# Kernel tuning notes

Measured on AMD Instinct MI355X. Metric: run time of the kernel, lower is better.

Reference implementation:

```python
import jax, jax.numpy as jnp
import numpy as np

EMBED = 256
HEADS = 8
SR = 2
RED = 2


def setup_inputs() -> dict:
    key = jax.random.key(0)
    ks = jax.random.split(key, 12)
    N, B, C = 1024, 64, EMBED
    inp = {
        "query": jax.random.normal(ks[0], (N, B, C), jnp.float32),
        "H": 32,
        "W": 32,
        "key": jax.random.normal(ks[1], (N, B, C), jnp.float32),
        "value": jax.random.normal(ks[2], (N, B, C), jnp.float32),
        # parameters
        "in_proj_weight": jax.random.normal(ks[3], (3 * C, C), jnp.float32) * (1.0 / np.sqrt(C)),
        "in_proj_bias": jnp.zeros((3 * C,), jnp.float32),
        "sr_w": jax.random.normal(ks[4], (C, C, SR, SR), jnp.float32) * np.sqrt(2.0 / (SR * SR * C)),
        "sr_b": jnp.zeros((C,), jnp.float32),
        "norm_g": jnp.ones((C,), jnp.float32),
        "norm_b": jnp.zeros((C,), jnp.float32),
        "out_w": jax.random.normal(ks[5], (C, C), jnp.float32) * (1.0 / np.sqrt(C)),
        "out_b": jnp.zeros((C,), jnp.float32),
        "se_w1": jax.random.normal(ks[6], (C // RED, C), jnp.float32) * 0.02,
        "se_w2": jax.random.normal(ks[7], (C, C // RED), jnp.float32) * 0.02,
    }
    return inp


def _angles(H, W):
    # get_index: a = (pi/2)*(i//W)/H, b = (pi/2)*(i%W)/W for flattened row-major index
    c = np.pi / 2
    idx = jnp.arange(H * W)
    a = c * (idx // W).astype(jnp.float32) / H
    b = c * (idx % W).astype(jnp.float32) / W
    return a, b


def _layernorm(x, g, b, eps=1e-5):
    mu = jnp.mean(x, -1, keepdims=True)
    var = jnp.mean(jnp.square(x - mu), -1, keepdims=True)
    return (x - mu) * jax.lax.rsqrt(var + eps) * g + b


def _abs_clamp(t, lo=1e-4, hi=1e4):
    return jnp.clip(jnp.abs(t), lo, hi) * jnp.sign(t)


def reference(query, H, W, key, value, in_proj_weight, in_proj_bias, sr_w, sr_b,
              norm_g, norm_b, out_w, out_b, se_w1, se_w2):
    N, B, C = query.shape
    h = HEADS
    hd = C // h
    scaling = hd ** (-0.5)

    x = jnp.transpose(query, (1, 0, 2))  # (B, N, C)

    # squeeze-excite gate from query: mean over tokens -> fc1 -> relu -> fc2 -> sigmoid
    se = jnp.mean(x, axis=1)                       # (B, C)
    se = jax.nn.sigmoid(jax.nn.relu(se @ se_w1.T) @ se_w2.T)  # (B, C)

    # spatial reduction conv (kernel=stride=sr_ratio) + layernorm for k/v source
    x_img = jnp.transpose(x, (0, 2, 1)).reshape(B, C, H, W)
    xr = jax.lax.conv_general_dilated(
        x_img, sr_w, window_strides=(SR, SR), padding="VALID",
        dimension_numbers=("NCHW", "OIHW", "NCHW"))
    xr = xr + sr_b[None, :, None, None]
    Hs, Ws = H // SR, W // SR
    Ns = Hs * Ws
    xr = jnp.transpose(xr.reshape(B, C, Ns), (0, 2, 1))  # (B, Ns, C)
    xr = _layernorm(xr, norm_g, norm_b)

    Wq, Wk, Wv = in_proj_weight[:C], in_proj_weight[C:2 * C], in_proj_weight[2 * C:]
    bq, bk, bv = in_proj_bias[:C], in_proj_bias[C:2 * C], in_proj_bias[2 * C:]

    def split_heads(t):  # (B, L, C) -> (B*h, L, hd)
        Bb, L, _ = t.shape
        return jnp.transpose(t.reshape(Bb, L, h, hd), (0, 2, 1, 3)).reshape(Bb * h, L, hd)

    q = split_heads((x @ Wq.T + bq) * scaling)
    k = split_heads(xr @ Wk.T + bk)
    v = split_heads(xr @ Wv.T + bv)

    q = jax.nn.relu(q)
    k = jax.nn.relu(k)

    # cosFormer-2d "sum" reweighting: cos(a_i - a_j) + cos(b_i - b_j)
    a, b = _angles(H, W)       # (N,)
    a2, b2 = _angles(Hs, Ws)   # (Ns,)

    def reweight(t, aa, bb):  # (BH, L, hd), angles (L,) -> (BH, L, 4*hd)
        aa = aa[None, :, None]
        bb = bb[None, :, None]
        return jnp.concatenate(
            [t * jnp.cos(aa), t * jnp.sin(aa), t * jnp.cos(bb), t * jnp.sin(bb)], axis=-1)

    q_ = reweight(q, a, b)     # (BH, N, 4hd)
    k_ = reweight(k, a2, b2)   # (BH, Ns, 4hd)

    # linear attention: never materialize the NxNs matrix
    kv = jnp.einsum("bnd,bnm->bdm", k_, v)             # (BH, 4hd, hd)
    denom = jnp.einsum("bnd,bd->bn", q_, k_.sum(1))    # (BH, N)
    denom = _abs_clamp(denom)
    attn = jnp.einsum("bnd,bdm->bnm", q_, kv) / denom[..., None]  # (BH, N, hd)

    attn = jnp.transpose(attn.reshape(B, h, N, hd), (0, 2, 1, 3)).reshape(B, N, C)
    out = attn @ out_w.T + out_b            # (B, N, C)
    out = out * se[:, None, :]              # SE channel gating
    return jnp.transpose(out, (1, 0, 2))    # (N, B, C)
```

## Files before the change

### kernel.cpp

```cpp
#include <hip/hip_runtime.h>

#define NTOK 1024
#define NB   64
#define CD   256
#define NHEAD 8
#define HDIM 32
#define NS 256
#define NBC 16384

typedef __attribute__((ext_vector_type(8))) short short8v;
typedef __attribute__((ext_vector_type(4))) short short4v;
typedef __attribute__((ext_vector_type(4))) float f32x4;

__device__ __forceinline__ unsigned bfr(float x){
  unsigned u = __float_as_uint(x);
  return (u + 0x7fffu + ((u>>16)&1u)) >> 16;
}
__device__ __forceinline__ void split2(float x, short &h, short &l){
  unsigned hu = bfr(x);
  float hf = __uint_as_float(hu << 16);
  unsigned lu = bfr(x - hf);
  h = (short)hu; l = (short)lu;
}

__global__ __launch_bounds__(256) void k_wcvt(const float* __restrict__ ipw, const float* __restrict__ ow,
                                              const float* __restrict__ srw,
                                              short* __restrict__ Wih, short* __restrict__ Wil,
                                              short* __restrict__ Woh, short* __restrict__ Wol,
                                              short* __restrict__ Wsh, short* __restrict__ Wsl){
  int u = blockIdx.x*256 + threadIdx.x;
  float xs[8];
  short* dh; short* dl; int dof;
  if (u < 24576){
    int n = u >> 5, off = (u & 31)*8;
    const float* s = ipw + n*CD + off;
    #pragma unroll
    for (int i=0;i<8;++i) xs[i] = s[i];
    dh = Wih; dl = Wil; dof = n*CD + off;
  } else if (u < 32768){
    int v = u - 24576;
    int n = v >> 5, off = (v & 31)*8;
    const float* s = ow + n*CD + off;
    #pragma unroll
    for (int i=0;i<8;++i) xs[i] = s[i];
    dh = Woh; dl = Wol; dof = n*CD + off;
  } else {
    int v = u - 32768;
    int n = v >> 7, koff = (v & 127)*8;
    int g = koff >> 8, cin0 = koff & 255;
    #pragma unroll
    for (int i=0;i<8;++i) xs[i] = srw[n*1024 + (cin0+i)*4 + g];
    dh = Wsh; dl = Wsl; dof = n*1024 + koff;
  }
  short8v h, l;
  #pragma unroll
  for (int i=0;i<8;++i){ short a,b; split2(xs[i],a,b); h[i]=a; l[i]=b; }
  *(short8v*)(dh + dof) = h;
  *(short8v*)(dl + dof) = l;
}

__global__ __launch_bounds__(256) void k_trig(float* __restrict__ t1, float* __restrict__ t2){
  int n = blockIdx.x*256 + threadIdx.x;
  const float c = 1.57079632679489662f;
  float aa = c * (float)(n >> 5) / 32.0f;
  float bb = c * (float)(n & 31) / 32.0f;
  t1[n*4+0]=cosf(aa); t1[n*4+1]=sinf(aa); t1[n*4+2]=cosf(bb); t1[n*4+3]=sinf(bb);
  if (n < 256){
    float a2 = c * (float)(n >> 4) / 16.0f;
    float b2 = c * (float)(n & 15) / 16.0f;
    t2[n*4+0]=cosf(a2); t2[n*4+1]=sinf(a2); t2[n*4+2]=cosf(b2); t2[n*4+3]=sinf(b2);
  }
}

__global__ __launch_bounds__(256) void k_semean(const float* __restrict__ q, float* __restrict__ part){
  int b = blockIdx.x >> 2, qr = blockIdx.x & 3;
  int c = threadIdx.x;
  const float* qp = q + (qr*256)*NBC + b*CD + c;
  float s0=0.f,s1=0.f,s2=0.f,s3=0.f;
  for (int n=0;n<256;n+=4){
    s0 += qp[(n  )*NBC];
    s1 += qp[(n+1)*NBC];
    s2 += qp[(n+2)*NBC];
    s3 += qp[(n+3)*NBC];
  }
  part[blockIdx.x*256 + c] = (s0+s1)+(s2+s3);
}

__global__ __launch_bounds__(256) void k_semlp(const float* __restrict__ part, const float* __restrict__ w1,
                                               const float* __restrict__ w2, float* __restrict__ se){
  __shared__ float sm[256];
  __shared__ float s1s[128];
  int b = blockIdx.x, t = threadIdx.x;
  float s = (part[(b*4+0)*256+t]+part[(b*4+1)*256+t])+(part[(b*4+2)*256+t]+part[(b*4+3)*256+t]);
  sm[t] = s*(1.0f/1024.0f);
  __syncthreads();
  if (t < 128){
    float a = 0.f;
    const float* wr = w1 + t*256;
    for (int c=0;c<256;c+=4){
      float4 wf = *(const float4*)(wr+c);
      a += sm[c]*wf.x + sm[c+1]*wf.y + sm[c+2]*wf.z + sm[c+3]*wf.w;
    }
    s1s[t] = fmaxf(a, 0.f);
  }
  __syncthreads();
  float a = 0.f;
  const float* wr2 = w2 + t*128;
  for (int c=0;c<128;c+=4){
    float4 wf = *(const float4*)(wr2+c);
    a += s1s[c]*wf.x + s1s[c+1]*wf.y + s1s[c+2]*wf.z + s1s[c+3]*wf.w;
  }
  se[b*256+t] = 1.0f/(1.0f+expf(-a));
}

__global__ __launch_bounds__(256) void k_conv(const float* __restrict__ qf,
                                              const short* __restrict__ Wsh, const short* __restrict__ Wsl,
                                              const float* __restrict__ srb, float* __restrict__ xr){
  __shared__ __align__(16) short Ah[64*32];
  __shared__ __align__(16) short Al[64*32];
  __shared__ __align__(16) short Bh[128*32];
  __shared__ __align__(16) short Bl[128*32];
  int mblk = blockIdx.x >> 1, nblk = blockIdx.x & 1;
  int m0 = mblk*64, n0 = nblk*128;
  int b = mblk >> 2;
  int pos0 = m0 & 255;
  int t = threadIdx.x, wave = t>>6, lane = t&63;
  int wm = wave>>1, wn = wave&1;
  int q = lane>>4, r = lane&15;
  int ra = t>>2, pa = (t&3)*8;
  int posA = pos0 + ra, hs = posA>>4, ws2 = posA&15;
  const f32x4 fz = {0.f,0.f,0.f,0.f};
  f32x4 acc[2][4];
  #pragma unroll
  for (int s=0;s<2;++s)
    #pragma unroll
    for (int tt=0;tt<4;++tt) acc[s][tt] = fz;
  for (int kc=0; kc<32; ++kc){
    int g = kc>>3, cin0 = (kc&7)*32;
    int gh = g>>1, gw = g&1;
    int tok = (2*hs+gh)*32 + 2*ws2 + gw;
    const float* src = qf + (size_t)tok*NBC + b*CD + cin0 + pa;
    float4 fa = *(const float4*)src;
    float4 fb = *(const float4*)(src+4);
    float xs[8] = {fa.x,fa.y,fa.z,fa.w,fb.x,fb.y,fb.z,fb.w};
    short8v hh, ll;
    #pragma unroll
    for (int i=0;i<8;++i){ short a0,b0; split2(xs[i],a0,b0); hh[i]=a0; ll[i]=b0; }
    *(short8v*)(Ah + ra*32 + pa) = hh;
    *(short8v*)(Al + ra*32 + pa) = ll;
    int ko = kc*32;
    #pragma unroll
    for (int rep=0; rep<2; ++rep){
      int rr = ra + rep*64;
      int gb = (n0 + rr)*1024 + ko + pa;
      *(short8v*)(Bh + rr*32 + pa) = *(const short8v*)(Wsh + gb);
      *(short8v*)(Bl + rr*32 + pa) = *(const short8v*)(Wsl + gb);
    }
    __syncthreads();
    short8v ah[2], al[2];
    #pragma unroll
    for (int s=0;s<2;++s){
      int row = wm*32 + s*16 + r;
      ah[s] = *(const short8v*)(Ah + row*32 + q*8);
      al[s] = *(const short8v*)(Al + row*32 + q*8);
    }
    #pragma unroll
    for (int tt=0;tt<4;++tt){
      int brow = wn*64 + tt*16 + r;
      short8v bh = *(const short8v*)(Bh + brow*32 + q*8);
      short8v bl = *(const short8v*)(Bl + brow*32 + q*8);
      #pragma unroll
      for (int s=0;s<2;++s){
        acc[s][tt] = __builtin_amdgcn_mfma_f32_16x16x32_bf16(ah[s], bh, acc[s][tt], 0,0,0);
        acc[s][tt] = __builtin_amdgcn_mfma_f32_16x16x32_bf16(ah[s], bl, acc[s][tt], 0,0,0);
        acc[s][tt] = __builtin_amdgcn_mfma_f32_16x16x32_bf16(al[s], bh, acc[s][tt], 0,0,0);
      }
    }
    __syncthreads();
  }
  #pragma unroll
  for (int s=0;s<2;++s){
    #pragma unroll
    for (int tt=0;tt<4;++tt){
      int c = n0 + wn*64 + tt*16 + r;
      float bias = srb[c];
      #pragma unroll
      for (int i=0;i<4;++i){
        int m = m0 + wm*32 + s*16 + q*4 + i;
        xr[m*CD + c] = acc[s][tt][i] + bias;
      }
    }
  }
}

__global__ __launch_bounds__(256) void k_ln(const float* __restrict__ xr, const float* __restrict__ g,
                                            const float* __restrict__ bta, short* __restrict__ Xh,
                                            short* __restrict__ Xl){
  int wv = threadIdx.x >> 6, lane = threadIdx.x & 63;
  int row = blockIdx.x*4 + wv;
  float4 v = ((const float4*)(xr + row*CD))[lane];
  float s = (v.x+v.y)+(v.z+v.w);
  #pragma unroll
  for (int off=1; off<64; off<<=1) s += __shfl_xor(s, off, 64);
  float mu = s * (1.0f/256.0f);
  float dx=v.x-mu, dy=v.y-mu, dz=v.z-mu, dw=v.w-mu;
  float s2 = (dx*dx+dy*dy)+(dz*dz+dw*dw);
  #pragma unroll
  for (int off=1; off<64; off<<=1) s2 += __shfl_xor(s2, off, 64);
  float inv = 1.0f / sqrtf(s2*(1.0f/256.0f) + 1e-5f);
  float4 gr = ((const float4*)g)[lane];
  float4 br = ((const float4*)bta)[lane];
  float o0 = dx*inv*gr.x + br.x;
  float o1 = dy*inv*gr.y + br.y;
  float o2 = dz*inv*gr.z + br.z;
  float o3 = dw*inv*gr.w + br.w;
  short4v h, l; short a0,b0;
  split2(o0,a0,b0); h[0]=a0; l[0]=b0;
  split2(o1,a0,b0); h[1]=a0; l[1]=b0;
  split2(o2,a0,b0); h[2]=a0; l[2]=b0;
  split2(o3,a0,b0); h[3]=a0; l[3]=b0;
  *(short4v*)(Xh + row*CD + lane*4) = h;
  *(short4v*)(Xl + row*CD + lane*4) = l;
}

__global__ __launch_bounds__(256) void k_qproj(const float* __restrict__ qf,
                                               const short* __restrict__ Wih, const short* __restrict__ Wil,
                                               const float* __restrict__ ipb,
                                               short* __restrict__ Qbh, short* __restrict__ Qbl){
  __shared__ __align__(16) short smem[16384];
  short* Ah = smem;
  short* Al = smem + 4096;
  short* Bh = smem + 8192;
  short* Bl = smem + 12288;
  int mblk = blockIdx.x >> 1, nblk = blockIdx.x & 1;
  int m0 = mblk*128, n0 = nblk*128;
  int t = threadIdx.x, wave = t>>6, lane = t&63;
  int wm = wave>>1, wn = wave&1;
  int q = lane>>4, r = lane&15;
  int cr = t>>2, cp = (t&3)*8;
  int cpS = (((t&3) ^ ((cr>>1)&3)))*8;
  int sw8 = ((r>>1)&3)*8;
  const f32x4 fz = {0.f,0.f,0.f,0.f};
  f32x4 acc[4][4];
  #pragma unroll
  for (int s=0;s<4;++s)
    #pragma unroll
    for (int tt=0;tt<4;++tt) acc[s][tt] = fz;
  for (int kc=0; kc<8; ++kc){
    int ko = kc*32;
    #pragma unroll
    for (int rep=0; rep<2; ++rep){
      int rr = cr + rep*64;
      int m = m0 + rr;
      const float* src = qf + (size_t)(m & 1023)*NBC + (m >> 10)*CD + ko + cp;
      float4 fa = *(const float4*)src;
      float4 fb = *(const float4*)(src+4);
      float xs[8] = {fa.x,fa.y,fa.z,fa.w,fb.x,fb.y,fb.z,fb.w};
      short8v hh, ll;
      #pragma unroll
      for (int i=0;i<8;++i){ short a0,b0; split2(xs[i],a0,b0); hh[i]=a0; ll[i]=b0; }
      *(short8v*)(Ah + rr*32 + cpS) = hh;
      *(short8v*)(Al + rr*32 + cpS) = ll;
      int gb = (n0 + rr)*CD + ko + cp;
      *(short8v*)(Bh + rr*32 + cpS) = *(const short8v*)(Wih + gb);
      *(short8v*)(Bl + rr*32 + cpS) = *(const short8v*)(Wil + gb);
    }
    __syncthreads();
    short8v ah[4], al[4];
    #pragma unroll
    for (int s=0;s<4;++s){
      int row = wm*64 + s*16 + r;
      ah[s] = *(const short8v*)(Ah + row*32 + ((q*8)^sw8));
      al[s] = *(const short8v*)(Al + row*32 + ((q*8)^sw8));
    }
    #pragma unroll
    for (int tt=0;tt<4;++tt){
      int brow = wn*64 + tt*16 + r;
      short8v bh = *(const short8v*)(Bh + brow*32 + ((q*8)^sw8));
      short8v bl = *(const short8v*)(Bl + brow*32 + ((q*8)^sw8));
      #pragma unroll
      for (int s=0;s<4;++s){
        acc[s][tt] = __builtin_amdgcn_mfma_f32_16x16x32_bf16(ah[s], bh, acc[s][tt], 0,0,0);
        acc[s][tt] = __builtin_amdgcn_mfma_f32_16x16x32_bf16(ah[s], bl, acc[s][tt], 0,0,0);
        acc[s][tt] = __builtin_amdgcn_mfma_f32_16x16x32_bf16(al[s], bh, acc[s][tt], 0,0,0);
      }
    }
    __syncthreads();
  }
  const float sc = 0.17677669529663687f;
  short* T = smem;
  #pragma unroll
  for (int s=0;s<4;++s){
    #pragma unroll
    for (int tt=0;tt<4;++tt){
      int c_loc = wn*64 + tt*16 + r;
      int chunk = c_loc >> 3, cb = c_loc & 7;
      float bias = ipb[n0 + c_loc];
      #pragma unroll
      for (int i=0;i<4;++i){
        int m_loc = wm*64 + s*16 + q*4 + i;
        float val = fmaxf(acc[s][tt][i] + bias, 0.f)*sc;
        unsigned hu = bfr(val);
        T[m_loc*128 + ((chunk ^ (m_loc&7))<<3) + cb] = (short)hu;
        acc[s][tt][i] = val - __uint_as_float(hu<<16);
      }
    }
  }
  __syncthreads();
  {
    int mrl = (lane>>2);
    int ccl = lane&3;
    #pragma unroll
    for (int e=0;e<8;++e){
      int hl = e&3, mg = e>>2;
      int m_loc = wave*32 + mg*16 + mrl;
      int cc16 = hl*4 + ccl;
      short8v v = *(const short8v*)(T + m_loc*128 + ((cc16 ^ (m_loc&7))<<3));
      *(short8v*)(Qbh + ((size_t)((n0>>5)+hl))*2097152 + (size_t)(m0+m_loc)*32 + ccl*8) = v;
    }
  }
  __syncthreads();
  #pragma unroll
  for (int s=0;s<4;++s){
    #pragma unroll
    for (int tt=0;tt<4;++tt){
      int c_loc = wn*64 + tt*16 + r;
      int chunk = c_loc >> 3, cb = c_loc & 7;
      #pragma unroll
      for (int i=0;i<4;++i){
        int m_loc = wm*64 + s*16 + q*4 + i;
        T[m_loc*128 + ((chunk ^ (m_loc&7))<<3) + cb] = (short)bfr(acc[s][tt][i]);
      }
    }
  }
  __syncthreads();
  {
    int mrl = (lane>>2);
    int ccl = lane&3;
    #pragma unroll
    for (int e=0;e<8;++e){
      int hl = e&3, mg = e>>2;
      int m_loc = wave*32 + mg*16 + mrl;
      int cc16 = hl*4 + ccl;
      short8v v = *(const short8v*)(T + m_loc*128 + ((cc16 ^ (m_loc&7))<<3));
      *(short8v*)(Qbl + ((size_t)((n0>>5)+hl))*2097152 + (size_t)(m0+m_loc)*32 + ccl*8) = v;
    }
  }
}

__global__ __launch_bounds__(256) void k_kvproj(const short* __restrict__ Xh, const short* __restrict__ Xl,
                                                const short* __restrict__ Wkh, const short* __restrict__ Wkl,
                                                const float* __restrict__ ipb, float* __restrict__ kb,
                                                float* __restrict__ vb){
  __shared__ __align__(16) short Ah[128*32];
  __shared__ __align__(16) short Al[128*32];
  __shared__ __align__(16) short Bh[128*32];
  __shared__ __align__(16) short Bl[128*32];
  int mblk = blockIdx.x >> 2, nblk = blockIdx.x & 3;
  int m0 = mblk*128, n0 = nblk*128;
  int t = threadIdx.x, wave = t>>6, lane = t&63;
  int wm = wave>>1, wn = wave&1;
  int q = lane>>4, r = lane&15;
  int cr = t>>2, cp = (t&3)*8;
  const f32x4 fz = {0.f,0.f,0.f,0.f};
  f32x4 acc[4][4];
  #pragma unroll
  for (int s=0;s<4;++s)
    #pragma unroll
    for (int tt=0;tt<4;++tt) acc[s][tt] = fz;
  for (int kc=0; kc<8; ++kc){
    int ko = kc*32;
    #pragma unroll
    for (int rep=0; rep<2; ++rep){
      int rr = cr + rep*64;
      int ga = (m0 + rr)*CD + ko + cp;
      *(short8v*)(Ah + rr*32 + cp) = *(const short8v*)(Xh + ga);
      *(short8v*)(Al + rr*32 + cp) = *(const short8v*)(Xl + ga);
      int gb = (n0 + rr)*CD + ko + cp;
      *(short8v*)(Bh + rr*32 + cp) = *(const short8v*)(Wkh + gb);
      *(short8v*)(Bl + rr*32 + cp) = *(const short8v*)(Wkl + gb);
    }
    __syncthreads();
    short8v ah[4], al[4];
    #pragma unroll
    for (int s=0;s<4;++s){
      int row = wm*64 + s*16 + r;
      ah[s] = *(const short8v*)(Ah + row*32 + q*8);
      al[s] = *(const short8v*)(Al + row*32 + q*8);
    }
    #pragma unroll
    for (int tt=0;tt<4;++tt){
      int brow = wn*64 + tt*16 + r;
      short8v bh = *(const short8v*)(Bh + brow*32 + q*8);
      short8v bl = *(const short8v*)(Bl + brow*32 + q*8);
      #pragma unroll
      for (int s=0;s<4;++s){
        acc[s][tt] = __builtin_amdgcn_mfma_f32_16x16x32_bf16(ah[s], bh, acc[s][tt], 0,0,0);
        acc[s][tt] = __builtin_amdgcn_mfma_f32_16x16x32_bf16(ah[s], bl, acc[s][tt], 0,0,0);
        acc[s][tt] = __builtin_amdgcn_mfma_f32_16x16x32_bf16(al[s], bh, acc[s][tt], 0,0,0);
      }
    }
    __syncthreads();
  }
  #pragma unroll
  for (int s=0;s<4;++s){
    #pragma unroll
    for (int tt=0;tt<4;++tt){
      int c = n0 + wn*64 + tt*16 + r;
      float bias = ipb[256 + c];
      #pragma unroll
      for (int i=0;i<4;++i){
        int m = m0 + wm*64 + s*16 + q*4 + i;
        float v = acc[s][tt][i] + bias;
        if (c < 256) kb[m*CD + c] = fmaxf(v, 0.f);
        else         vb[m*CD + (c-256)] = v;
      }
    }
  }
}

__global__ __launch_bounds__(256) void k_kv(const float* __restrict__ kb, const float* __restrict__ vbuf,
                                            const float* __restrict__ t2, short* __restrict__ Bhp,
                                            short* __restrict__ Blp){
  int bh = blockIdx.x; int b = bh >> 3, h = bh & 7;
  int t = threadIdx.x; int jq = t >> 5, m = t & 31;
  float acc[4][4];
  #pragma unroll
  for (int p=0;p<4;++p){ acc[p][0]=0.f; acc[p][1]=0.f; acc[p][2]=0.f; acc[p][3]=0.f; }
  const float* kbase = kb + h*HDIM + jq*4;
  const float* vbase = vbuf + h*HDIM + m;
  for (int n=0;n<256;++n){
    int ro = (b*NS + n)*CD;
    float4 k4 = *(const float4*)(kbase + ro);
    float vv = vbase[ro];
    float4 tt = *(const float4*)(t2 + n*4);
    float tv[4] = {tt.x, tt.y, tt.z, tt.w};
    float kk[4] = {k4.x, k4.y, k4.z, k4.w};
    #pragma unroll
    for (int p=0;p<4;++p){
      float tp = tv[p]*vv;
      #pragma unroll
      for (int jj=0;jj<4;++jj) acc[p][jj] += tp*kk[jj];
    }
  }
  short* bhb = Bhp + bh*4608;
  short* blb = Blp + bh*4608;
  #pragma unroll
  for (int p=0;p<4;++p){
    short4v h4, l4;
    #pragma unroll
    for (int jj=0;jj<4;++jj){ short a,bq; split2(acc[p][jj],a,bq); h4[jj]=a; l4[jj]=bq; }
    *(short4v*)(bhb + (p*32+m)*32 + jq*4) = h4;
    *(short4v*)(blb + (p*32+m)*32 + jq*4) = l4;
  }
  if (t < 128){
    int p = t >> 5, j = t & 31;
    float s=0.f;
    const float* kp = kb + h*HDIM + j;
    for (int n=0;n<256;++n) s += t2[n*4+p]*kp[(b*NS+n)*CD];
    short a,bq; split2(s,a,bq);
    bhb[(128+p)*32 + j] = a;
    blb[(128+p)*32 + j] = bq;
  } else {
    int idx = t - 128;
    #pragma unroll
    for (int ii=0;ii<3;++ii){
      bhb[4224 + idx*3 + ii] = 0;
      blb[4224 + idx*3 + ii] = 0;
    }
  }
}

__global__ __launch_bounds__(256) void k_attn(const short* __restrict__ Qbh, const short* __restrict__ Qbl,
                                              const short* __restrict__ Bhg, const short* __restrict__ Blg,
                                              const float* __restrict__ t1,
                                              short* __restrict__ Ath, short* __restrict__ Atl){
  __shared__ __align__(16) short Bh[144*32];
  __shared__ __align__(16) short Bl[144*32];
  __shared__ __align__(16) short Ah[256*32];
  __shared__ __align__(16) short Al[256*32];
  int bh = blockIdx.x, b = bh>>3, h = bh&7;
  int t = threadIdx.x, lane = t&63, wave = t>>6;
  int q = lane>>4, r = lane&15;
  {
    const short8v* sh = (const short8v*)(Bhg + bh*4608);
    const short8v* sl = (const short8v*)(Blg + bh*4608);
    for (int i=t; i<576; i+=256){
      ((short8v*)Bh)[i] = sh[i];
      ((short8v*)Bl)[i] = sl[i];
    }
  }
  __syncthreads();
  short8v bf_h[9], bf_l[9];
  #pragma unroll
  for (int nt=0; nt<9; ++nt){
    int row = nt*16 + r;
    bf_h[nt] = *(const short8v*)(Bh + row*32 + q*8);
    bf_l[nt] = *(const short8v*)(Bl + row*32 + q*8);
  }
  const short* qh_base = Qbh + ((size_t)h*65536 + (size_t)b*1024)*32;
  const short* ql_base = Qbl + ((size_t)h*65536 + (size_t)b*1024)*32;
  const f32x4 fz = {0.f,0.f,0.f,0.f};
  for (int u=0; u<4; ++u){
    __syncthreads();
    {
      const short8v* sh = (const short8v*)(qh_base + (u*256 + t)*32);
      const short8v* sl = (const short8v*)(ql_base + (u*256 + t)*32);
      short8v* dh = (short8v*)(Ah + t*32);
      short8v* dl = (short8v*)(Al + t*32);
      #pragma unroll
      for (int i=0;i<4;++i){ dh[i]=sh[i]; dl[i]=sl[i]; }
    }
    __syncthreads();
    #pragma unroll
    for (int mi=0; mi<4; ++mi){
      int mt = wave*4 + mi;
      short8v ah = *(const short8v*)(Ah + (mt*16 + r)*32 + q*8);
      short8v al = *(const short8v*)(Al + (mt*16 + r)*32 + q*8);
      f32x4 acc[9];
      #pragma unroll
      for (int nt=0;nt<9;++nt) acc[nt]=fz;
      #pragma unroll
      for (int nt=0;nt<9;++nt){
        acc[nt] = __builtin_amdgcn_mfma_f32_16x16x32_bf16(ah, bf_h[nt], acc[nt],0,0,0);
        acc[nt] = __builtin_amdgcn_mfma_f32_16x16x32_bf16(ah, bf_l[nt], acc[nt],0,0,0);
        acc[nt] = __builtin_amdgcn_mfma_f32_16x16x32_bf16(al, bf_h[nt], acc[nt],0,0,0);
      }
      int nbase = u*256 + mt*16 + q*4;
      int src = lane & 48;
      #pragma unroll
      for (int i=0;i<4;++i){
        int n = nbase + i;
        float4 tv = *(const float4*)(t1 + n*4);
        float dp0 = __shfl(acc[8][i], src+0, 64);
        float dp1 = __shfl(acc[8][i], src+1, 64);
        float dp2 = __shfl(acc[8][i], src+2, 64);
        float dp3 = __shfl(acc[8][i], src+3, 64);
        float den = tv.x*dp0 + tv.y*dp1 + tv.z*dp2 + tv.w*dp3;
        float a0 = tv.x*acc[0][i] + tv.y*acc[2][i] + tv.z*acc[4][i] + tv.w*acc[6][i];
        float a1 = tv.x*acc[1][i] + tv.y*acc[3][i] + tv.z*acc[5][i] + tv.w*acc[7][i];
        float sgn = (den>0.f) ? 1.f : ((den<0.f)? -1.f : 0.f);
        float ad = fminf(fmaxf(fabsf(den), 1e-4f), 1e4f);
// ... 54 lines not shown
    #pragma unroll
    for (int tt=0;tt<4;++tt){
      int brow = wn*64 + tt*16 + r;
      short8v bh = *(const short8v*)(Bh + brow*32 + q*8);
      short8v bl = *(const short8v*)(Bl + brow*32 + q*8);
      #pragma unroll
      for (int s=0;s<4;++s){
        acc[s][tt] = __builtin_amdgcn_mfma_f32_16x16x32_bf16(ah[s], bh, acc[s][tt], 0,0,0);
        acc[s][tt] = __builtin_amdgcn_mfma_f32_16x16x32_bf16(ah[s], bl, acc[s][tt], 0,0,0);
        acc[s][tt] = __builtin_amdgcn_mfma_f32_16x16x32_bf16(al[s], bh, acc[s][tt], 0,0,0);
      }
    }
    __syncthreads();
  }
  #pragma unroll
  for (int s=0;s<4;++s){
    #pragma unroll
    for (int tt=0;tt<4;++tt){
      int c = n0 + wn*64 + tt*16 + r;
      float bias = obv[c];
      #pragma unroll
      for (int i=0;i<4;++i){
        int m = m0 + wm*64 + s*16 + q*4 + i;
        int bb = m >> 10, ntok = m & 1023;
        float sev = se[bb*CD + c];
        dout[(ntok*NB + bb)*CD + c] = (acc[s][tt][i] + bias)*sev;
      }
    }
  }
}

extern "C" void kernel_launch(void* const* d_in, const int* in_sizes, int n_in,
                              void* d_out, int out_size, void* d_ws, size_t ws_size,
                              hipStream_t stream) {
  const float* query = (const float*)d_in[0];
  const float* ipw = (const float*)d_in[5];
  const float* ipb = (const float*)d_in[6];
  const float* srw = (const float*)d_in[7];
  const float* srb = (const float*)d_in[8];
  const float* ng  = (const float*)d_in[9];
  const float* nbb = (const float*)d_in[10];
  const float* ow  = (const float*)d_in[11];
  const float* obv = (const float*)d_in[12];
  const float* sw1 = (const float*)d_in[13];
  const float* sw2 = (const float*)d_in[14];
  float* dout = (float*)d_out;
  float* ws = (float*)d_ws;

  short* Qbh  = (short*)ws;
  short* Qbl  = (short*)(ws + 8388608);
  float* R1   = ws + 16777216;
  float* kb   = R1;
  float* vb   = R1 + 4194304;
  short* Ath  = (short*)R1;
  short* Atl  = (short*)(R1 + 8388608);
  float* xr   = ws + 33554432;
  short* Xh   = (short*)(ws + 37748736);
  short* Xl   = (short*)(ws + 39845888);
  short* kvbh = (short*)(ws + 41943040);
  short* kvbl = (short*)(ws + 43122688);
  float* part = ws + 44302336;
  float* se   = ws + 44367872;
  float* t1   = ws + 44384256;
  float* t2   = ws + 44388352;
  short* Wih  = (short*)(ws + 44389376);
  short* Wil  = (short*)(ws + 44487680);
  short* Woh  = (short*)(ws + 44585984);
  short* Wol  = (short*)(ws + 44618752);
  short* Wsh  = (short*)(ws + 44651520);
  short* Wsl  = (short*)(ws + 44782592);

  k_wcvt  <<<256,  256,0,stream>>>(ipw, ow, srw, Wih, Wil, Woh, Wol, Wsh, Wsl);
  k_trig  <<<4,    256,0,stream>>>(t1, t2);
  k_semean<<<256,  256,0,stream>>>(query, part);
  k_semlp <<<64,   256,0,stream>>>(part, sw1, sw2, se);
  k_conv  <<<512,  256,0,stream>>>(query, Wsh, Wsl, srb, xr);
  k_ln    <<<4096, 256,0,stream>>>(xr, ng, nbb, Xh, Xl);
  k_qproj <<<1024, 256,0,stream>>>(query, Wih, Wil, ipb, Qbh, Qbl);
  k_kvproj<<<512,  256,0,stream>>>(Xh, Xl, Wih + 256*CD, Wil + 256*CD, ipb, kb, vb);
  k_kv    <<<512,  256,0,stream>>>(kb, vb, t2, kvbh, kvbl);
  k_attn  <<<512,  256,0,stream>>>(Qbh, Qbl, kvbh, kvbl, t1, Ath, Atl);
  k_outproj<<<1024,256,0,stream>>>(Ath, Atl, Woh, Wol, obv, se, dout);
}
```

Before: 458.3 us.

## Merge independent kernels into combined launches and fuse kv build into attention

Groups the independent stages (weight conversion, trig tables, SE mean) into one launch, and the conv, Q projection and SE MLP into another, using block-index dispatch. The kv-state computation now runs inside the attention kernel and writes straight to shared memory, which removes a global round trip and one launch. Workspace buffers are remapped so Ath/Atl no longer alias kb/vb, since those are now read in the same kernel. Block-index dispatch gives each launch a mix of very different block types and shared-memory sizes, which can hurt occupancy and load balance.

```diff
diff --git a/kernel.cpp b/kernel.cpp
--- a/kernel.cpp
+++ b/kernel.cpp
@@ -23,173 +23,300 @@
   h = (short)hu; l = (short)lu;
 }
 
-__global__ __launch_bounds__(256) void k_wcvt(const float* __restrict__ ipw, const float* __restrict__ ow,
-                                              const float* __restrict__ srw,
-                                              short* __restrict__ Wih, short* __restrict__ Wil,
-                                              short* __restrict__ Woh, short* __restrict__ Wol,
-                                              short* __restrict__ Wsh, short* __restrict__ Wsl){
-  int u = blockIdx.x*256 + threadIdx.x;
-  float xs[8];
-  short* dh; short* dl; int dof;
-  if (u < 24576){
-    int n = u >> 5, off = (u & 31)*8;
-    const float* s = ipw + n*CD + off;
-    #pragma unroll
-    for (int i=0;i<8;++i) xs[i] = s[i];
-    dh = Wih; dl = Wil; dof = n*CD + off;
-  } else if (u < 32768){
-    int v = u - 24576;
-    int n = v >> 5, off = (v & 31)*8;
-    const float* s = ow + n*CD + off;
-    #pragma unroll
-    for (int i=0;i<8;++i) xs[i] = s[i];
-    dh = Woh; dl = Wol; dof = n*CD + off;
+__global__ __launch_bounds__(256) void k_pre(const float* __restrict__ ipw, const float* __restrict__ ow,
+                                             const float* __restrict__ srw,
+                                             short* __restrict__ Wih, short* __restrict__ Wil,
+                                             short* __restrict__ Woh, short* __restrict__ Wol,
+                                             short* __restrict__ Wsh, short* __restrict__ Wsl,
+                                             float* __restrict__ t1, float* __restrict__ t2,
+                                             const float* __restrict__ query, float* __restrict__ part){
+  int bid = blockIdx.x, t = threadIdx.x;
+  if (bid < 256){
+    int u = bid*256 + t;
+    float xs[8];
+    short* dh; short* dl; int dof;
+    if (u < 24576){
+      int n = u >> 5, off = (u & 31)*8;
+      const float* s = ipw + n*CD + off;
+      #pragma unroll
+      for (int i=0;i<8;++i) xs[i] = s[i];
+      dh = Wih; dl = Wil; dof = n*CD + off;
+    } else if (u < 32768){
+      int v = u - 24576;
+      int n = v >> 5, off = (v & 31)*8;
+      const float* s = ow + n*CD + off;
+      #pragma unroll
+      for (int i=0;i<8;++i) xs[i] = s[i];
+      dh = Woh; dl = Wol; dof = n*CD + off;
+    } else {
+      int v = u - 32768;
+      int n = v >> 7, koff = (v & 127)*8;
+      int g = koff >> 8, cin0 = koff & 255;
+      #pragma unroll
+      for (int i=0;i<8;++i) xs[i] = srw[n*1024 + (cin0+i)*4 + g];
+      dh = Wsh; dl = Wsl; dof = n*1024 + koff;
+    }
+    short8v h, l;
+    #pragma unroll
+    for (int i=0;i<8;++i){ short a,b; split2(xs[i],a,b); h[i]=a; l[i]=b; }
+    *(short8v*)(dh + dof) = h;
+    *(short8v*)(dl + dof) = l;
+  } else if (bid < 260){
+    int n = (bid-256)*256 + t;
+    const float c = 1.57079632679489662f;
+    float aa = c * (float)(n >> 5) / 32.0f;
+    float bb = c * (float)(n & 31) / 32.0f;
+    t1[n*4+0]=cosf(aa); t1[n*4+1]=sinf(aa); t1[n*4+2]=cosf(bb); t1[n*4+3]=sinf(bb);
+    if (n < 256){
+      float a2 = c * (float)(n >> 4) / 16.0f;
+      float b2 = c * (float)(n & 15) / 16.0f;
+      t2[n*4+0]=cosf(a2); t2[n*4+1]=sinf(a2); t2[n*4+2]=cosf(b2); t2[n*4+3]=sinf(b2);
+    }
   } else {
-    int v = u - 32768;
-    int n = v >> 7, koff = (v & 127)*8;
-    int g = koff >> 8, cin0 = koff & 255;
-    #pragma unroll
-    for (int i=0;i<8;++i) xs[i] = srw[n*1024 + (cin0+i)*4 + g];
-    dh = Wsh; dl = Wsl; dof = n*1024 + koff;
-  }
-  short8v h, l;
-  #pragma unroll
-  for (int i=0;i<8;++i){ short a,b; split2(xs[i],a,b); h[i]=a; l[i]=b; }
-  *(short8v*)(dh + dof) = h;
-  *(short8v*)(dl + dof) = l;
-}
-
-__global__ __launch_bounds__(256) void k_trig(float* __restrict__ t1, float* __restrict__ t2){
-  int n = blockIdx.x*256 + threadIdx.x;
-  const float c = 1.57079632679489662f;
-  float aa = c * (float)(n >> 5) / 32.0f;
-  float bb = c * (float)(n & 31) / 32.0f;
-  t1[n*4+0]=cosf(aa); t1[n*4+1]=sinf(aa); t1[n*4+2]=cosf(bb); t1[n*4+3]=sinf(bb);
-  if (n < 256){
-    float a2 = c * (float)(n >> 4) / 16.0f;
-    float b2 = c * (float)(n & 15) / 16.0f;
-    t2[n*4+0]=cosf(a2); t2[n*4+1]=sinf(a2); t2[n*4+2]=cosf(b2); t2[n*4+3]=sinf(b2);
-  }
-}
-
-__global__ __launch_bounds__(256) void k_semean(const float* __restrict__ q, float* __restrict__ part){
-  int b = blockIdx.x >> 2, qr = blockIdx.x & 3;
-  int c = threadIdx.x;
-  const float* qp = q + (qr*256)*NBC + b*CD + c;
-  float s0=0.f,s1=0.f,s2=0.f,s3=0.f;
-  for (int n=0;n<256;n+=4){
-    s0 += qp[(n  )*NBC];
-    s1 += qp[(n+1)*NBC];
-    s2 += qp[(n+2)*NBC];
-    s3 += qp[(n+3)*NBC];
-  }
-  part[blockIdx.x*256 + c] = (s0+s1)+(s2+s3);
-}
-
-__global__ __launch_bounds__(256) void k_semlp(const float* __restrict__ part, const float* __restrict__ w1,
-                                               const float* __restrict__ w2, float* __restrict__ se){
-  __shared__ float sm[256];
-  __shared__ float s1s[128];
-  int b = blockIdx.x, t = threadIdx.x;
-  float s = (part[(b*4+0)*256+t]+part[(b*4+1)*256+t])+(part[(b*4+2)*256+t]+part[(b*4+3)*256+t]);
-  sm[t] = s*(1.0f/1024.0f);
-  __syncthreads();
-  if (t < 128){
+    int vb_ = bid - 260;
+    int b = vb_ >> 2, qr = vb_ & 3;
+    const float* qp = query + (qr*256)*NBC + b*CD + t;
+    float s0=0.f,s1=0.f,s2=0.f,s3=0.f;
+    for (int n=0;n<256;n+=4){
+      s0 += qp[(n  )*NBC];
+      s1 += qp[(n+1)*NBC];
+      s2 += qp[(n+2)*NBC];
+      s3 += qp[(n+3)*NBC];
+    }
+    part[vb_*256 + t] = (s0+s1)+(s2+s3);
+  }
+}
+
+__global__ __launch_bounds__(256) void k_mid(const float* __restrict__ qf,
+                                             const short* __restrict__ Wsh, const short* __restrict__ Wsl,
+                                             const float* __restrict__ srb, float* __restrict__ xr,
+                                             const short* __restrict__ Wih, const short* __restrict__ Wil,
+                                             const float* __restrict__ ipb,
+                                             short* __restrict__ Qbh, short* __restrict__ Qbl,
+                                             const float* __restrict__ part, const float* __restrict__ w1,
+                                             const float* __restrict__ w2, float* __restrict__ se){
+  __shared__ __align__(16) short smem[16384];
+  int bid = blockIdx.x, t = threadIdx.x;
+  if (bid < 512){
+    short* Ah = smem;
+    short* Al = smem + 2048;
+    short* Bh = smem + 4096;
+    short* Bl = smem + 8192;
+    int mblk = bid >> 1, nblk = bid & 1;
+    int m0 = mblk*64, n0 = nblk*128;
+    int b = mblk >> 2;
+    int pos0 = m0 & 255;
+    int wave = t>>6, lane = t&63;
+    int wm = wave>>1, wn = wave&1;
+    int q = lane>>4, r = lane&15;
+    int ra = t>>2, pa = (t&3)*8;
+    int posA = pos0 + ra, hs = posA>>4, ws2 = posA&15;
+    const f32x4 fz = {0.f,0.f,0.f,0.f};
+    f32x4 acc[2][4];
+    #pragma unroll
+    for (int s=0;s<2;++s)
+      #pragma unroll
+      for (int tt=0;tt<4;++tt) acc[s][tt] = fz;
+    for (int kc=0; kc<32; ++kc){
+      int g = kc>>3, cin0 = (kc&7)*32;
+      int gh = g>>1, gw = g&1;
+      int tok = (2*hs+gh)*32 + 2*ws2 + gw;
+      const float* src = qf + (size_t)tok*NBC + b*CD + cin0 + pa;
+      float4 fa = *(const float4*)src;
+      float4 fb = *(const float4*)(src+4);
+      float xs[8] = {fa.x,fa.y,fa.z,fa.w,fb.x,fb.y,fb.z,fb.w};
+      short8v hh, ll;
+      #pragma unroll
+      for (int i=0;i<8;++i){ short a0,b0; split2(xs[i],a0,b0); hh[i]=a0; ll[i]=b0; }
+      *(short8v*)(Ah + ra*32 + pa) = hh;
+      *(short8v*)(Al + ra*32 + pa) = ll;
+      int ko = kc*32;
+      #pragma unroll
+      for (int rep=0; rep<2; ++rep){
+        int rr = ra + rep*64;
+        int gb = (n0 + rr)*1024 + ko + pa;
+        *(short8v*)(Bh + rr*32 + pa) = *(const short8v*)(Wsh + gb);
+        *(short8v*)(Bl + rr*32 + pa) = *(const short8v*)(Wsl + gb);
+      }
+      __syncthreads();
+      short8v ah[2], al[2];
+      #pragma unroll
+      for (int s=0;s<2;++s){
+        int row = wm*32 + s*16 + r;
+        ah[s] = *(const short8v*)(Ah + row*32 + q*8);
+        al[s] = *(const short8v*)(Al + row*32 + q*8);
+      }
+      #pragma unroll
+      for (int tt=0;tt<4;++tt){
+        int brow = wn*64 + tt*16 + r;
+        short8v bh = *(const short8v*)(Bh + brow*32 + q*8);
+        short8v bl = *(const short8v*)(Bl + brow*32 + q*8);
+        #pragma unroll
+        for (int s=0;s<2;++s){
+          acc[s][tt] = __builtin_amdgcn_mfma_f32_16x16x32_bf16(ah[s], bh, acc[s][tt], 0,0,0);
+          acc[s][tt] = __builtin_amdgcn_mfma_f32_16x16x32_bf16(ah[s], bl, acc[s][tt], 0,0,0);
+          acc[s][tt] = __builtin_amdgcn_mfma_f32_16x16x32_bf16(al[s], bh, acc[s][tt], 0,0,0);
+        }
+      }
+      __syncthreads();
+    }
+    #pragma unroll
+    for (int s=0;s<2;++s){
+      #pragma unroll
+      for (int tt=0;tt<4;++tt){
+        int c = n0 + wn*64 + tt*16 + r;
+        float bias = srb[c];
+        #pragma unroll
+        for (int i=0;i<4;++i){
+          int m = m0 + wm*32 + s*16 + q*4 + i;
+          xr[m*CD + c] = acc[s][tt][i] + bias;
+        }
+      }
+    }
+  } else if (bid < 1536){
+    short* Ah = smem;
+    short* Al = smem + 4096;
+    short* Bh = smem + 8192;
+    short* Bl = smem + 12288;
+    int qb_ = bid - 512;
+    int mblk = qb_ >> 1, nblk = qb_ & 1;
+    int m0 = mblk*128, n0 = nblk*128;
+    int wave = t>>6, lane = t&63;
+    int wm = wave>>1, wn = wave&1;
+    int q = lane>>4, r = lane&15;
+    int cr = t>>2, cp = (t&3)*8;
+    int cpS = (((t&3) ^ ((cr>>1)&3)))*8;
+    int sw8 = ((r>>1)&3)*8;
+    const f32x4 fz = {0.f,0.f,0.f,0.f};
+    f32x4 acc[4][4];
+    #pragma unroll
+    for (int s=0;s<4;++s)
+      #pragma unroll
+      for (int tt=0;tt<4;++tt) acc[s][tt] = fz;
+    for (int kc=0; kc<8; ++kc){
+      int ko = kc*32;
+      #pragma unroll
+      for (int rep=0; rep<2; ++rep){
+        int rr = cr + rep*64;
+        int m = m0 + rr;
+        const float* src = qf + (size_t)(m & 1023)*NBC + (m >> 10)*CD + ko + cp;
+        float4 fa = *(const float4*)src;
+        float4 fb = *(const float4*)(src+4);
+        float xs[8] = {fa.x,fa.y,fa.z,fa.w,fb.x,fb.y,fb.z,fb.w};
+        short8v hh, ll;
+        #pragma unroll
+        for (int i=0;i<8;++i){ short a0,b0; split2(xs[i],a0,b0); hh[i]=a0; ll[i]=b0; }
+        *(short8v*)(Ah + rr*32 + cpS) = hh;
+        *(short8v*)(Al + rr*32 + cpS) = ll;
+        int gb = (n0 + rr)*CD + ko + cp;
+        *(short8v*)(Bh + rr*32 + cpS) = *(const short8v*)(Wih + gb);
+        *(short8v*)(Bl + rr*32 + cpS) = *(const short8v*)(Wil + gb);
+      }
+      __syncthreads();
+      short8v ah[4], al[4];
+      #pragma unroll
+      for (int s=0;s<4;++s){
+        int row = wm*64 + s*16 + r;
+        ah[s] = *(const short8v*)(Ah + row*32 + ((q*8)^sw8));
+        al[s] = *(const short8v*)(Al + row*32 + ((q*8)^sw8));
+      }
+      #pragma unroll
+      for (int tt=0;tt<4;++tt){
+        int brow = wn*64 + tt*16 + r;
+        short8v bh = *(const short8v*)(Bh + brow*32 + ((q*8)^sw8));
+        short8v bl = *(const short8v*)(Bl + brow*32 + ((q*8)^sw8));
+        #pragma unroll
+        for (int s=0;s<4;++s){
+          acc[s][tt] = __builtin_amdgcn_mfma_f32_16x16x32_bf16(ah[s], bh, acc[s][tt], 0,0,0);
+          acc[s][tt] = __builtin_amdgcn_mfma_f32_16x16x32_bf16(ah[s], bl, acc[s][tt], 0,0,0);
+          acc[s][tt] = __builtin_amdgcn_mfma_f32_16x16x32_bf16(al[s], bh, acc[s][tt], 0,0,0);
+        }
+      }
+      __syncthreads();
+    }
+    const float sc = 0.17677669529663687f;
+    short* T = smem;
+    #pragma unroll
+    for (int s=0;s<4;++s){
+      #pragma unroll
+      for (int tt=0;tt<4;++tt){
+        int c_loc = wn*64 + tt*16 + r;
+        int chunk = c_loc >> 3, cb = c_loc & 7;
+        float bias = ipb[n0 + c_loc];
+        #pragma unroll
+        for (int i=0;i<4;++i){
+          int m_loc = wm*64 + s*16 + q*4 + i;
+          float val = fmaxf(acc[s][tt][i] + bias, 0.f)*sc;
+          unsigned hu = bfr(val);
+          T[m_loc*128 + ((chunk ^ (m_loc&7))<<3) + cb] = (short)hu;
+          acc[s][tt][i] = val - __uint_as_float(hu<<16);
+        }
+      }
+    }
+    __syncthreads();
+    {
+      int mrl = (lane>>2);
+      int ccl = lane&3;
+      #pragma unroll
+      for (int e=0;e<8;++e){
+        int hl = e&3, mg = e>>2;
+        int m_loc = wave*32 + mg*16 + mrl;
+        int cc16 = hl*4 + ccl;
+        short8v v = *(const short8v*)(T + m_loc*128 + ((cc16 ^ (m_loc&7))<<3));
+        *(short8v*)(Qbh + ((size_t)((n0>>5)+hl))*2097152 + (size_t)(m0+m_loc)*32 + ccl*8) = v;
+      }
+    }
+    __syncthreads();
+    #pragma unroll
+    for (int s=0;s<4;++s){
+      #pragma unroll
+      for (int tt=0;tt<4;++tt){
+        int c_loc = wn*64 + tt*16 + r;
+        int chunk = c_loc >> 3, cb = c_loc & 7;
+        #pragma unroll
+        for (int i=0;i<4;++i){
+          int m_loc = wm*64 + s*16 + q*4 + i;
+          T[m_loc*128 + ((chunk ^ (m_loc&7))<<3) + cb] = (short)bfr(acc[s][tt][i]);
+        }
+      }
+    }
+    __syncthreads();
+    {
+      int mrl = (lane>>2);
+      int ccl = lane&3;
+      #pragma unroll
+      for (int e=0;e<8;++e){
+        int hl = e&3, mg = e>>2;
+        int m_loc = wave*32 + mg*16 + mrl;
+        int cc16 = hl*4 + ccl;
+        short8v v = *(const short8v*)(T + m_loc*128 + ((cc16 ^ (m_loc&7))<<3));
+        *(short8v*)(Qbl + ((size_t)((n0>>5)+hl))*2097152 + (size_t)(m0+m_loc)*32 + ccl*8) = v;
+      }
+    }
+  } else {
+    float* sm = (float*)smem;
+    float* s1s = sm + 256;
+    int b = bid - 1536;
+    float s = (part[(b*4+0)*256+t]+part[(b*4+1)*256+t])+(part[(b*4+2)*256+t]+part[(b*4+3)*256+t]);
+    sm[t] = s*(1.0f/1024.0f);
+    __syncthreads();
+    if (t < 128){
+      float a = 0.f;
+      const float* wr = w1 + t*256;
+      for (int c=0;c<256;c+=4){
+        float4 wf = *(const float4*)(wr+c);
+        a += sm[c]*wf.x + sm[c+1]*wf.y + sm[c+2]*wf.z + sm[c+3]*wf.w;
+      }
+      s1s[t] = fmaxf(a, 0.f);
+    }
+    __syncthreads();
     float a = 0.f;
-    const float* wr = w1 + t*256;
-    for (int c=0;c<256;c+=4){
-      float4 wf = *(const float4*)(wr+c);
-      a += sm[c]*wf.x + sm[c+1]*wf.y + sm[c+2]*wf.z + sm[c+3]*wf.w;
-    }
-    s1s[t] = fmaxf(a, 0.f);
-  }
-  __syncthreads();
-  float a = 0.f;
-  const float* wr2 = w2 + t*128;
-  for (int c=0;c<128;c+=4){
-    float4 wf = *(const float4*)(wr2+c);
-    a += s1s[c]*wf.x + s1s[c+1]*wf.y + s1s[c+2]*wf.z + s1s[c+3]*wf.w;
-  }
-  se[b*256+t] = 1.0f/(1.0f+expf(-a));
-}
-
-__global__ __launch_bounds__(256) void k_conv(const float* __restrict__ qf,
-                                              const short* __restrict__ Wsh, const short* __restrict__ Wsl,
-                                              const float* __restrict__ srb, float* __restrict__ xr){
-  __shared__ __align__(16) short Ah[64*32];
-  __shared__ __align__(16) short Al[64*32];
-  __shared__ __align__(16) short Bh[128*32];
-  __shared__ __align__(16) short Bl[128*32];
-  int mblk = blockIdx.x >> 1, nblk = blockIdx.x & 1;
-  int m0 = mblk*64, n0 = nblk*128;
-  int b = mblk >> 2;
-  int pos0 = m0 & 255;
-  int t = threadIdx.x, wave = t>>6, lane = t&63;
-  int wm = wave>>1, wn = wave&1;
-  int q = lane>>4, r = lane&15;
-  int ra = t>>2, pa = (t&3)*8;
-  int posA = pos0 + ra, hs = posA>>4, ws2 = posA&15;
-  const f32x4 fz = {0.f,0.f,0.f,0.f};
-  f32x4 acc[2][4];
-  #pragma unroll
-  for (int s=0;s<2;++s)
-    #pragma unroll
-    for (int tt=0;tt<4;++tt) acc[s][tt] = fz;
-  for (int kc=0; kc<32; ++kc){
-    int g = kc>>3, cin0 = (kc&7)*32;
-    int gh = g>>1, gw = g&1;
-    int tok = (2*hs+gh)*32 + 2*ws2 + gw;
-    const float* src = qf + (size_t)tok*NBC + b*CD + cin0 + pa;
-    float4 fa = *(const float4*)src;
-    float4 fb = *(const float4*)(src+4);
-    float xs[8] = {fa.x,fa.y,fa.z,fa.w,fb.x,fb.y,fb.z,fb.w};
-    short8v hh, ll;
-    #pragma unroll
-    for (int i=0;i<8;++i){ short a0,b0; split2(xs[i],a0,b0); hh[i]=a0; ll[i]=b0; }
-    *(short8v*)(Ah + ra*32 + pa) = hh;
-    *(short8v*)(Al + ra*32 + pa) = ll;
-    int ko = kc*32;
-    #pragma unroll
-    for (int rep=0; rep<2; ++rep){
-      int rr = ra + rep*64;
-      int gb = (n0 + rr)*1024 + ko + pa;
-      *(short8v*)(Bh + rr*32 + pa) = *(const short8v*)(Wsh + gb);
-      *(short8v*)(Bl + rr*32 + pa) = *(const short8v*)(Wsl + gb);
-    }
-    __syncthreads();
-    short8v ah[2], al[2];
-    #pragma unroll
-    for (int s=0;s<2;++s){
-      int row = wm*32 + s*16 + r;
-      ah[s] = *(const short8v*)(Ah + row*32 + q*8);
-      al[s] = *(const short8v*)(Al + row*32 + q*8);
-    }
-    #pragma unroll
-    for (int tt=0;tt<4;++tt){
-      int brow = wn*64 + tt*16 + r;
-      short8v bh = *(const short8v*)(Bh + brow*32 + q*8);
-      short8v bl = *(const short8v*)(Bl + brow*32 + q*8);
-      #pragma unroll
-      for (int s=0;s<2;++s){
-        acc[s][tt] = __builtin_amdgcn_mfma_f32_16x16x32_bf16(ah[s], bh, acc[s][tt], 0,0,0);
-        acc[s][tt] = __builtin_amdgcn_mfma_f32_16x16x32_bf16(ah[s], bl, acc[s][tt], 0,0,0);
-        acc[s][tt] = __builtin_amdgcn_mfma_f32_16x16x32_bf16(al[s], bh, acc[s][tt], 0,0,0);
-      }
-    }
-    __syncthreads();
-  }
-  #pragma unroll
-  for (int s=0;s<2;++s){
-    #pragma unroll
-    for (int tt=0;tt<4;++tt){
-      int c = n0 + wn*64 + tt*16 + r;
-      float bias = srb[c];
-      #pragma unroll
-      for (int i=0;i<4;++i){
-        int m = m0 + wm*32 + s*16 + q*4 + i;
-        xr[m*CD + c] = acc[s][tt][i] + bias;
-      }
-    }
+    const float* wr2 = w2 + t*128;
+    for (int c=0;c<128;c+=4){
+      float4 wf = *(const float4*)(wr2+c);
+      a += s1s[c]*wf.x + s1s[c+1]*wf.y + s1s[c+2]*wf.z + s1s[c+3]*wf.w;
+    }
+    se[b*256+t] = 1.0f/(1.0f+expf(-a));
   }
 }
 
@@ -223,131 +350,6 @@
   *(short4v*)(Xl + row*CD + lane*4) = l;
 }
 
-__global__ __launch_bounds__(256) void k_qproj(const float* __restrict__ qf,
-                                               const short* __restrict__ Wih, const short* __restrict__ Wil,
-                                               const float* __restrict__ ipb,
-                                               short* __restrict__ Qbh, short* __restrict__ Qbl){
-  __shared__ __align__(16) short smem[16384];
-  short* Ah = smem;
-  short* Al = smem + 4096;
-  short* Bh = smem + 8192;
-  short* Bl = smem + 12288;
-  int mblk = blockIdx.x >> 1, nblk = blockIdx.x & 1;
-  int m0 = mblk*128, n0 = nblk*128;
-  int t = threadIdx.x, wave = t>>6, lane = t&63;
-  int wm = wave>>1, wn = wave&1;
-  int q = lane>>4, r = lane&15;
-  int cr = t>>2, cp = (t&3)*8;
-  int cpS = (((t&3) ^ ((cr>>1)&3)))*8;
-  int sw8 = ((r>>1)&3)*8;
-  const f32x4 fz = {0.f,0.f,0.f,0.f};
-  f32x4 acc[4][4];
-  #pragma unroll
-  for (int s=0;s<4;++s)
-    #pragma unroll
-    for (int tt=0;tt<4;++tt) acc[s][tt] = fz;
-  for (int kc=0; kc<8; ++kc){
-    int ko = kc*32;
-    #pragma unroll
-    for (int rep=0; rep<2; ++rep){
-      int rr = cr + rep*64;
-      int m = m0 + rr;
-      const float* src = qf + (size_t)(m & 1023)*NBC + (m >> 10)*CD + ko + cp;
-      float4 fa = *(const float4*)src;
-      float4 fb = *(const float4*)(src+4);
-      float xs[8] = {fa.x,fa.y,fa.z,fa.w,fb.x,fb.y,fb.z,fb.w};
-      short8v hh, ll;
-      #pragma unroll
-      for (int i=0;i<8;++i){ short a0,b0; split2(xs[i],a0,b0); hh[i]=a0; ll[i]=b0; }
-      *(short8v*)(Ah + rr*32 + cpS) = hh;
-      *(short8v*)(Al + rr*32 + cpS) = ll;
-      int gb = (n0 + rr)*CD + ko + cp;
-      *(short8v*)(Bh + rr*32 + cpS) = *(const short8v*)(Wih + gb);
-      *(short8v*)(Bl + rr*32 + cpS) = *(const short8v*)(Wil + gb);
-    }
-    __syncthreads();
-    short8v ah[4], al[4];
-    #pragma unroll
-    for (int s=0;s<4;++s){
-      int row = wm*64 + s*16 + r;
-      ah[s] = *(const short8v*)(Ah + row*32 + ((q*8)^sw8));
-      al[s] = *(const short8v*)(Al + row*32 + ((q*8)^sw8));
-    }
-    #pragma unroll
-    for (int tt=0;tt<4;++tt){
-      int brow = wn*64 + tt*16 + r;
-      short8v bh = *(const short8v*)(Bh + brow*32 + ((q*8)^sw8));
-      short8v bl = *(const short8v*)(Bl + brow*32 + ((q*8)^sw8));
-      #pragma unroll
-      for (int s=0;s<4;++s){
-        acc[s][tt] = __builtin_amdgcn_mfma_f32_16x16x32_bf16(ah[s], bh, acc[s][tt], 0,0,0);
-        acc[s][tt] = __builtin_amdgcn_mfma_f32_16x16x32_bf16(ah[s], bl, acc[s][tt], 0,0,0);
-        acc[s][tt] = __builtin_amdgcn_mfma_f32_16x16x32_bf16(al[s], bh, acc[s][tt], 0,0,0);
-      }
-    }
-    __syncthreads();
-  }
-  const float sc = 0.17677669529663687f;
-  short* T = smem;
-  #pragma unroll
-  for (int s=0;s<4;++s){
-    #pragma unroll
-    for (int tt=0;tt<4;++tt){
-      int c_loc = wn*64 + tt*16 + r;
-      int chunk = c_loc >> 3, cb = c_loc & 7;
-      float bias = ipb[n0 + c_loc];
-      #pragma unroll
-      for (int i=0;i<4;++i){
-        int m_loc = wm*64 + s*16 + q*4 + i;
-        float val = fmaxf(acc[s][tt][i] + bias, 0.f)*sc;
-        unsigned hu = bfr(val);
-        T[m_loc*128 + ((chunk ^ (m_loc&7))<<3) + cb] = (short)hu;
-        acc[s][tt][i] = val - __uint_as_float(hu<<16);
-      }
-    }
-  }
-  __syncthreads();
-  {
-    int mrl = (lane>>2);
-    int ccl = lane&3;
-    #pragma unroll
-    for (int e=0;e<8;++e){
-      int hl = e&3, mg = e>>2;
-      int m_loc = wave*32 + mg*16 + mrl;
-      int cc16 = hl*4 + ccl;
-      short8v v = *(const short8v*)(T + m_loc*128 + ((cc16 ^ (m_loc&7))<<3));
-      *(short8v*)(Qbh + ((size_t)((n0>>5)+hl))*2097152 + (size_t)(m0+m_loc)*32 + ccl*8) = v;
-    }
-  }
-  __syncthreads();
-  #pragma unroll
-  for (int s=0;s<4;++s){
-    #pragma unroll
-    for (int tt=0;tt<4;++tt){
-      int c_loc = wn*64 + tt*16 + r;
-      int chunk = c_loc >> 3, cb = c_loc & 7;
-      #pragma unroll
-      for (int i=0;i<4;++i){
-        int m_loc = wm*64 + s*16 + q*4 + i;
-        T[m_loc*128 + ((chunk ^ (m_loc&7))<<3) + cb] = (short)bfr(acc[s][tt][i]);
-      }
-    }
-  }
-  __syncthreads();
-  {
-    int mrl = (lane>>2);
-    int ccl = lane&3;
-    #pragma unroll
-    for (int e=0;e<8;++e){
-      int hl = e&3, mg = e>>2;
-      int m_loc = wave*32 + mg*16 + mrl;
-      int cc16 = hl*4 + ccl;
-      short8v v = *(const short8v*)(T + m_loc*128 + ((cc16 ^ (m_loc&7))<<3));
-      *(short8v*)(Qbl + ((size_t)((n0>>5)+hl))*2097152 + (size_t)(m0+m_loc)*32 + ccl*8) = v;
-    }
-  }
-}
-
 __global__ __launch_bounds__(256) void k_kvproj(const short* __restrict__ Xh, const short* __restrict__ Xl,
                                                 const short* __restrict__ Wkh, const short* __restrict__ Wkl,
                                                 const float* __restrict__ ipb, float* __restrict__ kb,
@@ -419,62 +421,11 @@
   }
 }
 
-__global__ __launch_bounds__(256) void k_kv(const float* __restrict__ kb, const float* __restrict__ vbuf,
-                                            const float* __restrict__ t2, short* __restrict__ Bhp,
-                                            short* __restrict__ Blp){
-  int bh = blockIdx.x; int b = bh >> 3, h = bh & 7;
-  int t = threadIdx.x; int jq = t >> 5, m = t & 31;
-  float acc[4][4];
-  #pragma unroll
-  for (int p=0;p<4;++p){ acc[p][0]=0.f; acc[p][1]=0.f; acc[p][2]=0.f; acc[p][3]=0.f; }
-  const float* kbase = kb + h*HDIM + jq*4;
-  const float* vbase = vbuf + h*HDIM + m;
-  for (int n=0;n<256;++n){
-    int ro = (b*NS + n)*CD;
-    float4 k4 = *(const float4*)(kbase + ro);
-    float vv = vbase[ro];
-    float4 tt = *(const float4*)(t2 + n*4);
-    float tv[4] = {tt.x, tt.y, tt.z, tt.w};
-    float kk[4] = {k4.x, k4.y, k4.z, k4.w};
-    #pragma unroll
-    for (int p=0;p<4;++p){
-      float tp = tv[p]*vv;
-      #pragma unroll
-      for (int jj=0;jj<4;++jj) acc[p][jj] += tp*kk[jj];
-    }
-  }
-  short* bhb = Bhp + bh*4608;
-  short* blb = Blp + bh*4608;
-  #pragma unroll
-  for (int p=0;p<4;++p){
-    short4v h4, l4;
-    #pragma unroll
-    for (int jj=0;jj<4;++jj){ short a,bq; split2(acc[p][jj],a,bq); h4[jj]=a; l4[jj]=bq; }
-    *(short4v*)(bhb + (p*32+m)*32 + jq*4) = h4;
-    *(short4v*)(blb + (p*32+m)*32 + jq*4) = l4;
-  }
-  if (t < 128){
-    int p = t >> 5, j = t & 31;
-    float s=0.f;
-    const float* kp = kb + h*HDIM + j;
-    for (int n=0;n<256;++n) s += t2[n*4+p]*kp[(b*NS+n)*CD];
-    short a,bq; split2(s,a,bq);
-    bhb[(128+p)*32 + j] = a;
-    blb[(128+p)*32 + j] = bq;
-  } else {
-    int idx = t - 128;
-    #pragma unroll
-    for (int ii=0;ii<3;++ii){
-      bhb[4224 + idx*3 + ii] = 0;
-      blb[4224 + idx*3 + ii] = 0;
-    }
-  }
-}
-
-__global__ __launch_bounds__(256) void k_attn(const short* __restrict__ Qbh, const short* __restrict__ Qbl,
-                                              const short* __restrict__ Bhg, const short* __restrict__ Blg,
-                                              const float* __restrict__ t1,
-                                              short* __restrict__ Ath, short* __restrict__ Atl){
+__global__ __launch_bounds__(256) void k_kvattn(const float* __restrict__ kb, const float* __restrict__ vbuf,
+                                                const float* __restrict__ t2,
+                                                const short* __restrict__ Qbh, const short* __restrict__ Qbl,
+                                                const float* __restrict__ t1,
+                                                short* __restrict__ Ath, short* __restrict__ Atl){
   __shared__ __align__(16) short Bh[144*32];
   __shared__ __align__(16) short Bl[144*32];
   __shared__ __align__(16) short Ah[256*32];
@@ -483,11 +434,49 @@
   int t = threadIdx.x, lane = t&63, wave = t>>6;
   int q = lane>>4, r = lane&15;
   {
-    const short8v* sh = (const short8v*)(Bhg + bh*4608);
-    const short8v* sl = (const short8v*)(Blg + bh*4608);
-    for (int i=t; i<576; i+=256){
-      ((short8v*)Bh)[i] = sh[i];
-      ((short8v*)Bl)[i] = sl[i];
+    int jq = t >> 5, m = t & 31;
+    float acc[4][4];
+    #pragma unroll
+    for (int p=0;p<4;++p){ acc[p][0]=0.f; acc[p][1]=0.f; acc[p][2]=0.f; acc[p][3]=0.f; }
+    const float* kbase = kb + h*HDIM + jq*4;
+    const float* vbase = vbuf + h*HDIM + m;
+    for (int n=0;n<256;++n){
+      int ro = (b*NS + n)*CD;
+      float4 k4 = *(const float4*)(kbase + ro);
+      float vv = vbase[ro];
+      float4 tt = *(const float4*)(t2 + n*4);
+      float tv[4] = {tt.x, tt.y, tt.z, tt.w};
+      float kk[4] = {k4.x, k4.y, k4.z, k4.w};
+      #pragma unroll
+      for (int p=0;p<4;++p){
+        float tp = tv[p]*vv;
+        #pragma unroll
+        for (int jj=0;jj<4;++jj) acc[p][jj] += tp*kk[jj];
+      }
+    }
+    #pragma unroll
+    for (int p=0;p<4;++p){
+      short4v h4, l4;
+      #pragma unroll
+      for (int jj=0;jj<4;++jj){ short a,bq; split2(acc[p][jj],a,bq); h4[jj]=a; l4[jj]=bq; }
+      *(short4v*)(Bh + (p*32+m)*32 + jq*4) = h4;
+      *(short4v*)(Bl + (p*32+m)*32 + jq*4) = l4;
+    }
+    if (t < 128){
+      int p = t >> 5, j = t & 31;
+      float s=0.f;
+      const float* kp = kb + h*HDIM + j;
+      for (int n=0;n<256;++n) s += t2[n*4+p]*kp[(b*NS+n)*CD];
+      short a,bq; split2(s,a,bq);
+      Bh[(128+p)*32 + j] = a;
+      Bl[(128+p)*32 + j] = bq;
+    } else {
+      int idx = t - 128;
+      #pragma unroll
+      for (int ii=0;ii<3;++ii){
+        Bh[4224 + idx*3 + ii] = 0;
+        Bl[4224 + idx*3 + ii] = 0;
+      }
     }
   }
   __syncthreads();
@@ -648,13 +637,11 @@
   float* R1   = ws + 16777216;
   float* kb   = R1;
   float* vb   = R1 + 4194304;
-  short* Ath  = (short*)R1;
-  short* Atl  = (short*)(R1 + 8388608);
+  short* Ath  = (short*)(R1 + 8388608);
+  short* Atl  = (short*)(ws + 33554432);
   float* xr   = ws + 33554432;
   short* Xh   = (short*)(ws + 37748736);
   short* Xl   = (short*)(ws + 39845888);
-  short* kvbh = (short*)(ws + 41943040);
-  short* kvbl = (short*)(ws + 43122688);
   float* part = ws + 44302336;
   float* se   = ws + 44367872;
   float* t1   = ws + 44384256;
@@ -666,15 +653,10 @@
   short* Wsh  = (short*)(ws + 44651520);
   short* Wsl  = (short*)(ws + 44782592);
 
-  k_wcvt  <<<256,  256,0,stream>>>(ipw, ow, srw, Wih, Wil, Woh, Wol, Wsh, Wsl);
-  k_trig  <<<4,    256,0,stream>>>(t1, t2);
-  k_semean<<<256,  256,0,stream>>>(query, part);
-  k_semlp <<<64,   256,0,stream>>>(part, sw1, sw2, se);
-  k_conv  <<<512,  256,0,stream>>>(query, Wsh, Wsl, srb, xr);
+  k_pre   <<<516,  256,0,stream>>>(ipw, ow, srw, Wih, Wil, Woh, Wol, Wsh, Wsl, t1, t2, query, part);
+  k_mid   <<<1600, 256,0,stream>>>(query, Wsh, Wsl, srb, xr, Wih, Wil, ipb, Qbh, Qbl, part, sw1, sw2, se);
   k_ln    <<<4096, 256,0,stream>>>(xr, ng, nbb, Xh, Xl);
-  k_qproj <<<1024, 256,0,stream>>>(query, Wih, Wil, ipb, Qbh, Qbl);
   k_kvproj<<<512,  256,0,stream>>>(Xh, Xl, Wih + 256*CD, Wil + 256*CD, ipb, kb, vb);
-  k_kv    <<<512,  256,0,stream>>>(kb, vb, t2, kvbh, kvbl);
-  k_attn  <<<512,  256,0,stream>>>(Qbh, Qbl, kvbh, kvbl, t1, Ath, Atl);
+  k_kvattn<<<512,  256,0,stream>>>(kb, vb, t2, Qbh, Qbl, t1, Ath, Atl);
   k_outproj<<<1024,256,0,stream>>>(Ath, Atl, Woh, Wol, obv, se, dout);
 }
```

Measured after the change: 430.0 us. 6.2% less time.
